# Kernel optimization log

Hardware: AMD Instinct MI355X
Metric: run time of the kernel (lower is better)

Reference implementation:

```python
import jax, jax.numpy as jnp
import numpy as np

B, H, WD, C = 16, 96, 96, 256
WS, SH, NH = 6, 3, 8
N = WS * WS
ALPHA = (2 * 6) ** 0.25  # deepnorm alpha, n_layers=6
SCALE = (C // NH) ** 0.5  # faithful to source: head_dim**0.5 (not **-0.5)
EPS = 1e-5


def _rel_index(ws):
    coords = np.stack(np.meshgrid(np.arange(ws), np.arange(ws), indexing='ij'))  # (2,ws,ws)
    flat = coords.reshape(2, -1)
    rel = (flat[:, :, None] - flat[:, None, :]).transpose(1, 2, 0).copy()
    rel[..., 0] += ws - 1
    rel[..., 1] += ws - 1
    rel[..., 0] *= 2 * ws - 1
    return jnp.asarray(rel.sum(-1))  # (N,N) int


def _attn_mask(h, w, ws, sh):
    img = np.zeros((h, w))
    cnt = 0
    for hs in (slice(0, -ws), slice(-ws, -sh), slice(-sh, None)):
        for wsl in (slice(0, -ws), slice(-ws, -sh), slice(-sh, None)):
            img[hs, wsl] = cnt
            cnt += 1
    win = img.reshape(h // ws, ws, w // ws, ws).transpose(0, 2, 1, 3).reshape(-1, ws * ws)
    diff = win[:, None, :] - win[:, :, None]
    return jnp.asarray(np.where(diff != 0, -100.0, 0.0), jnp.float32)  # (nW,N,N)


def _ln(t, w, b):
    mu = jnp.mean(t, -1, keepdims=True)
    var = jnp.var(t, -1, keepdims=True)
    return (t - mu) * jax.lax.rsqrt(var + EPS) * w + b


def setup_inputs() -> dict:
    key = jax.random.key(0)
    ks = jax.random.split(key, 8)
    d = {
        'x': jax.random.normal(ks[0], (B, H * WD, C), jnp.float32),
        'qkv_w': jax.random.normal(ks[1], (C, 3 * C), jnp.float32) * 0.02,
        'qkv_b': jnp.zeros((3 * C,), jnp.float32),
        'bias_table': jax.random.normal(ks[2], ((2 * WS - 1) ** 2, NH), jnp.float32) * 0.02,
        'proj_w': jax.random.normal(ks[3], (C, C), jnp.float32) * 0.02,
        'proj_b': jnp.zeros((C,), jnp.float32),
        'norm1_w': jnp.ones((C,), jnp.float32),
        'norm1_b': jnp.zeros((C,), jnp.float32),
        'norm2_w': jnp.ones((C,), jnp.float32),
        'norm2_b': jnp.zeros((C,), jnp.float32),
        'fc1_w': jax.random.normal(ks[4], (C, 4 * C), jnp.float32) * 0.02,
        'fc1_b': jnp.zeros((4 * C,), jnp.float32),
        'fc2_w': jax.random.normal(ks[5], (4 * C, C), jnp.float32) * 0.02,
        'fc2_b': jnp.zeros((C,), jnp.float32),
    }
    return d


def reference(x, qkv_w, qkv_b, bias_table, proj_w, proj_b, norm1_w, norm1_b,
              norm2_w, norm2_b, fc1_w, fc1_b, fc2_w, fc2_b):
    hd = C // NH
    nW = (H // WS) * (WD // WS)
    shortcut = x  # (B, L, C), norm_before=False -> post-norm
    xs = x.reshape(B, H, WD, C)
    xs = jnp.roll(xs, (-SH, -SH), axis=(1, 2))  # cyclic shift
    # window partition -> (B*nW, N, C)
    xw = xs.reshape(B, H // WS, WS, WD // WS, WS, C).transpose(0, 1, 3, 2, 4, 5).reshape(B * nW, N, C)
    qkv = (xw @ qkv_w + qkv_b).reshape(B * nW, N, 3, NH, hd).transpose(2, 0, 3, 1, 4)
    q, k, v = qkv[0] * SCALE, qkv[1], qkv[2]
    attn = jnp.einsum('bhnd,bhmd->bhnm', q, k)  # (B*nW, H, N, N)
    bias = bias_table[_rel_index(WS).reshape(-1)].reshape(N, N, NH).transpose(2, 0, 1)
    attn = attn + bias[None]
    mask = _attn_mask(H, WD, WS, SH)  # (nW, N, N)
    attn = attn.reshape(B, nW, NH, N, N) + mask[None, :, None]
    attn = jax.nn.softmax(attn.reshape(B * nW, NH, N, N), axis=-1)
    out = jnp.einsum('bhnm,bhmd->bhnd', attn, v).transpose(0, 2, 1, 3).reshape(B * nW, N, C)
    out = out @ proj_w + proj_b
    # faithful buggy window_reverse: identity permute == plain reshape
    xs = out.reshape(B, H // WS, WS, WD // WS, WS, C).reshape(B, H, WD, C)
    xs = jnp.roll(xs, (SH, SH), axis=(1, 2))
    x1 = _ln(shortcut * ALPHA + xs.reshape(B, H * WD, C), norm1_w, norm1_b)
    hmid = jax.nn.gelu(x1 @ fc1_w + fc1_b, approximate=False)
    x2 = _ln(x1 * ALPHA + (hmid @ fc2_w + fc2_b), norm2_w, norm2_b)
    return x2
```

## Files before the change

### kernel.cpp

```cpp
#include <hip/hip_runtime.h>
#include <math.h>

typedef __bf16 bf16x8 __attribute__((ext_vector_type(8)));
typedef __bf16 bf16x4 __attribute__((ext_vector_type(4)));
typedef short  s16x4  __attribute__((ext_vector_type(4)));
typedef float  f32x4  __attribute__((ext_vector_type(4)));

#define NTOK 147456
#define LTOK 9216
#define ALPHA 1.8612097182041991f
#define QSCALE 5.656854249492380196f
#define MFMA32(a,b,c) __builtin_amdgcn_mfma_f32_16x16x32_bf16((a),(b),(c),0,0,0)
#define SWB(row,kb) ((kb) ^ ((row)&7))

__device__ __forceinline__ f32x4 MFMA16(bf16x4 a, bf16x4 b, f32x4 c) {
#if __has_builtin(__builtin_amdgcn_mfma_f32_16x16x16bf16_1k)
    return __builtin_amdgcn_mfma_f32_16x16x16bf16_1k(*(s16x4*)&a, *(s16x4*)&b, c, 0, 0, 0);
#else
    f32x4 d = c;
    asm volatile("s_nop 1\n\ts_nop 1\n\t"
                 "v_mfma_f32_16x16x16_bf16 %0, %1, %2, %0\n\t"
                 "s_nop 7\n\ts_nop 7"
                 : "+v"(d) : "v"(a), "v"(b));
    return d;
#endif
}

__device__ __forceinline__ float gelu_sig(float x) {
    const float e = __expf(-1.702f * x);
    return x * __builtin_amdgcn_rcpf(1.0f + e);
}

__device__ __forceinline__ void gll16(const void* g, void* l) {
    __builtin_amdgcn_global_load_lds(
        (const __attribute__((address_space(1))) void*)g,
        (__attribute__((address_space(3))) void*)l, 16, 0, 0);
}

__global__ __launch_bounds__(256) void k0_prep(
    const float* __restrict__ qkv_w, const float* __restrict__ proj_w,
    const float* __restrict__ fc1_w, const float* __restrict__ fc2_w,
    const float* __restrict__ bias_table,
    __bf16* __restrict__ qkvT, __bf16* __restrict__ projT,
    __bf16* __restrict__ w1T, __bf16* __restrict__ w2T,
    float* __restrict__ bmask)
{
    const int id = blockIdx.x * 256 + threadIdx.x;
    if (id < 196608) {
        const int o = id >> 8, k = id & 255;
        qkvT[id] = (__bf16)qkv_w[k * 768 + o];
    } else if (id < 262144) {
        const int i = id - 196608, o = i >> 8, k = i & 255;
        projT[i] = (__bf16)proj_w[k * 256 + o];
    } else if (id < 524288) {
        const int i = id - 262144, o = i >> 8, k = i & 255;
        w1T[i] = (__bf16)fc1_w[k * 1024 + o];
    } else if (id < 786432) {
        const int i = id - 524288, o = i >> 10, k = i & 1023;
        w2T[i] = (__bf16)fc2_w[k * 256 + o];
    } else if (id < 860160) {
        const int e = id - 786432;
        const int m = e % 48;
        const int n = (e / 48) % 48;
        const int h = (e / 2304) % 8;
        const int ty = e / 18432;
        const int nn = n < 36 ? n : 35, mm = m < 36 ? m : 35;
        const int i1 = nn / 6, j1 = nn - i1 * 6;
        const int i2 = mm / 6, j2 = mm - i2 * 6;
        float v = bias_table[((i1 - i2 + 5) * 11 + (j1 - j2 + 5)) * 8 + h];
        const int hg1 = (ty & 2) ? (i1 < 3 ? 1 : 2) : 0;
        const int wg1 = (ty & 1) ? (j1 < 3 ? 1 : 2) : 0;
        const int hg2 = (ty & 2) ? (i2 < 3 ? 1 : 2) : 0;
        const int wg2 = (ty & 1) ? (j2 < 3 ? 1 : 2) : 0;
        if (hg1 * 3 + wg1 != hg2 * 3 + wg2) v -= 100.0f;
        if (m >= 36) v = -1e30f;
        bmask[e] = v;
    }
}

__global__ __launch_bounds__(512, 4) void k1f_qkv_attn(
    const float* __restrict__ x, const __bf16* __restrict__ qkvT,
    const float* __restrict__ qkv_b, const float* __restrict__ bmask,
    __bf16* __restrict__ attnout)
{
    __shared__ __attribute__((aligned(16))) __bf16 As[48][256];
    __shared__ int srcrow[48];

    const int t = threadIdx.x;
    const int wid = t >> 6, lane = t & 63;
    const int l15 = lane & 15, lg = lane >> 4;
    const int blk = blockIdx.x;
    const int win = blk & 255;
    const int wh = win >> 4, ww = win & 15;
    const int h = wid;

    if (t < 48) {
        int n = t; if (n > 35) n = 35;
        const int b = blk >> 8;
        const int gh = (wh * 6 + n / 6 + 3) % 96;
        const int gw = (ww * 6 + n % 6 + 3) % 96;
        srcrow[t] = b * LTOK + gh * 96 + gw;
    }
    __syncthreads();

    for (int o = t; o < 48 * 32; o += 512) {
        const int row = o >> 5, kb = o & 31;
        const float* src = x + (size_t)srcrow[row] * 256 + kb * 8;
        const float4 f0 = *(const float4*)src;
        const float4 f1 = *(const float4*)(src + 4);
        bf16x8 p;
        p[0] = (__bf16)f0.x; p[1] = (__bf16)f0.y; p[2] = (__bf16)f0.z; p[3] = (__bf16)f0.w;
        p[4] = (__bf16)f1.x; p[5] = (__bf16)f1.y; p[6] = (__bf16)f1.z; p[7] = (__bf16)f1.w;
        *(bf16x8*)&As[row][SWB(row, kb) * 8] = p;
    }
    __syncthreads();

    const f32x4 fzero = {0.f, 0.f, 0.f, 0.f};
    f32x4 accQ[2][3], accK[2][3], accV[2][3];
    #pragma unroll
    for (int c = 0; c < 2; ++c)
        #pragma unroll
        for (int r = 0; r < 3; ++r) { accQ[c][r] = fzero; accK[c][r] = fzero; accV[c][r] = fzero; }

    const __bf16* bbase = qkvT + (size_t)(h * 32 + l15) * 256 + lg * 8;

    for (int kc = 0; kc < 8; ++kc) {
        bf16x8 af[3];
        #pragma unroll
        for (int rt = 0; rt < 3; ++rt) {
            const int ar = rt * 16 + l15;
            af[rt] = *(const bf16x8*)&As[ar][SWB(ar, kc * 4 + lg) * 8];
        }
        #pragma unroll
        for (int ct = 0; ct < 2; ++ct) {
            const __bf16* bp = bbase + (size_t)ct * 16 * 256 + kc * 32;
            const bf16x8 bq = *(const bf16x8*)bp;
            const bf16x8 bk = *(const bf16x8*)(bp + 65536);
            const bf16x8 bv = *(const bf16x8*)(bp + 131072);
            #pragma unroll
            for (int rt = 0; rt < 3; ++rt) {
                accQ[ct][rt] = MFMA32(bq, af[rt], accQ[ct][rt]);
                accK[ct][rt] = MFMA32(bk, af[rt], accK[ct][rt]);
                accV[ct][rt] = MFMA32(af[rt], bv, accV[ct][rt]);
            }
        }
    }

    bf16x4 qf[3][2], kf[3][2];
    bf16x4 vf[2][3];
    #pragma unroll
    for (int dh = 0; dh < 2; ++dh) {
        #pragma unroll
        for (int q = 0; q < 4; ++q) {
            const float qb = qkv_b[h * 32 + dh * 16 + lg * 4 + q];
            const float kb = qkv_b[256 + h * 32 + dh * 16 + lg * 4 + q];
            #pragma unroll
            for (int rt = 0; rt < 3; ++rt) {
                qf[rt][dh][q] = (__bf16)((accQ[dh][rt][q] + qb) * QSCALE);
                kf[rt][dh][q] = (__bf16)(accK[dh][rt][q] + kb);
            }
        }
    }
    #pragma unroll
    for (int cd = 0; cd < 2; ++cd) {
        const float vb = qkv_b[512 + h * 32 + cd * 16 + l15];
        #pragma unroll
        for (int c3 = 0; c3 < 3; ++c3)
            #pragma unroll
            for (int q = 0; q < 4; ++q)
                vf[cd][c3][q] = (__bf16)(accV[cd][c3][q] + vb);
    }

    f32x4 s[3][3];
    #pragma unroll
    for (int qt = 0; qt < 3; ++qt)
        #pragma unroll
        for (int c3 = 0; c3 < 3; ++c3) {
            f32x4 acc = MFMA16(kf[c3][0], qf[qt][0], fzero);
            s[qt][c3] = MFMA16(kf[c3][1], qf[qt][1], acc);
        }

    const int ty = ((wh == 15) ? 2 : 0) + ((ww == 15) ? 1 : 0);
    const float* bmp = bmask + (size_t)(ty * 8 + h) * 2304;
    bf16x4 pa[3][3];
    #pragma unroll
    for (int qt = 0; qt < 3; ++qt) {
        const float* brow = bmp + (qt * 16 + l15) * 48 + lg * 4;
        const float4 b0 = *(const float4*)brow;
        const float4 b1 = *(const float4*)(brow + 16);
        const float4 b2 = *(const float4*)(brow + 32);
        float vals[3][4];
        #pragma unroll
        for (int q = 0; q < 4; ++q) {
            vals[0][q] = s[qt][0][q] + ((const float*)&b0)[q];
            vals[1][q] = s[qt][1][q] + ((const float*)&b1)[q];
            vals[2][q] = s[qt][2][q] + ((const float*)&b2)[q];
        }
        float mx = -1e30f;
        #pragma unroll
        for (int c3 = 0; c3 < 3; ++c3)
            #pragma unroll
            for (int q = 0; q < 4; ++q) mx = fmaxf(mx, vals[c3][q]);
        mx = fmaxf(mx, __shfl_xor(mx, 16));
        mx = fmaxf(mx, __shfl_xor(mx, 32));
        float sum = 0.f;
        #pragma unroll
        for (int c3 = 0; c3 < 3; ++c3)
            #pragma unroll
            for (int q = 0; q < 4; ++q) {
                const float e = __expf(vals[c3][q] - mx);
                vals[c3][q] = e;
                sum += e;
            }
        sum += __shfl_xor(sum, 16);
        sum += __shfl_xor(sum, 32);
        const float inv = 1.0f / sum;
        #pragma unroll
        for (int c3 = 0; c3 < 3; ++c3)
            #pragma unroll
            for (int q = 0; q < 4; ++q)
                pa[qt][c3][q] = (__bf16)(vals[c3][q] * inv);
    }

    const size_t rowbase = (size_t)blk * 36;
    #pragma unroll
    for (int qt = 0; qt < 3; ++qt)
        #pragma unroll
        for (int cd = 0; cd < 2; ++cd) {
            f32x4 o = MFMA16(pa[qt][0], vf[cd][0], fzero);
            o = MFMA16(pa[qt][1], vf[cd][1], o);
            o = MFMA16(pa[qt][2], vf[cd][2], o);
            #pragma unroll
            for (int q = 0; q < 4; ++q) {
                const int n = qt * 16 + lg * 4 + q;
                if (n < 36)
                    attnout[(rowbase + n) * 256 + h * 32 + cd * 16 + l15] = (__bf16)o[q];
            }
        }
}

__global__ __launch_bounds__(512) void k2_proj_ln(
    const __bf16* __restrict__ attnout, const __bf16* __restrict__ projT,
    const float* __restrict__ proj_b, const float* __restrict__ x,
    const float* __restrict__ n1w, const float* __restrict__ n1b,
    __bf16* __restrict__ x1b)
{
    __shared__ __attribute__((aligned(16))) __bf16 As[128][64];
    __shared__ __attribute__((aligned(16))) __bf16 Bs[256][64];
    __shared__ float ps[128][4], ps2[128][4];
    const int t = threadIdx.x;
    const int wid = t >> 6, lane = t & 63;
    const int l15 = lane & 15, lg = lane >> 4;
    const int mb = blockIdx.x;
    const int wm = wid >> 2, wn = wid & 3;

    const f32x4 fzero = {0.f, 0.f, 0.f, 0.f};
    f32x4 acc[4][4];
    #pragma unroll
    for (int i = 0; i < 4; ++i)
        #pragma unroll
        for (int j = 0; j < 4; ++j) acc[i][j] = fzero;

    for (int kc = 0; kc < 4; ++kc) {
        __syncthreads();
        #pragma unroll
        for (int i = 0; i < 2; ++i) {
            const int r0 = wid * 16 + i * 8;
            const int row = r0 + (lane >> 3), kbl = lane & 7;
            gll16(attnout + (size_t)(mb * 128 + row) * 256 + kc * 64 + ((kbl ^ (row & 7)) * 8),
                  &As[r0][0]);
        }
        #pragma unroll
        for (int i = 0; i < 4; ++i) {
            const int r0 = wid * 32 + i * 8;
            const int row = r0 + (lane >> 3), kbl = lane & 7;
            gll16(projT + (size_t)row * 256 + kc * 64 + ((kbl ^ (row & 7)) * 8),
                  &Bs[r0][0]);
        }
        __syncthreads();
        #pragma unroll
        for (int kk = 0; kk < 2; ++kk) {
            bf16x8 af[4], bfr[4];
            #pragma unroll
            for (int rt = 0; rt < 4; ++rt) {
                const int ar = wm * 64 + rt * 16 + l15;
                af[rt] = *(const bf16x8*)&As[ar][((kk * 4 + lg) ^ (ar & 7)) * 8];
            }
            #pragma unroll
            for (int ct = 0; ct < 4; ++ct) {
                const int br = wn * 64 + ct * 16 + l15;
                bfr[ct] = *(const bf16x8*)&Bs[br][((kk * 4 + lg) ^ (br & 7)) * 8];
            }
            #pragma unroll
            for (int rt = 0; rt < 4; ++rt)
                #pragma unroll
                for (int ct = 0; ct < 4; ++ct)
                    acc[rt][ct] = MFMA32(af[rt], bfr[ct], acc[rt][ct]);
        }
    }

    int dtok_[4][4];
    #pragma unroll
    for (int rt = 0; rt < 4; ++rt) {
        #pragma unroll
        for (int q = 0; q < 4; ++q) {
            const int rowl = wm * 64 + rt * 16 + lg * 4 + q;
            const int tok = mb * 128 + rowl;
            const int b = tok / LTOK, l = tok % LTOK;
            const int hh = l / 96, wwp = l % 96;
            const int dtok = b * LTOK + ((hh + 3) % 96) * 96 + ((wwp + 3) % 96);
            dtok_[rt][q] = dtok;
            float s = 0.f, s2 = 0.f;
            #pragma unroll
            for (int ct = 0; ct < 4; ++ct) {
                const int col = wn * 64 + ct * 16 + l15;
                const float v = acc[rt][ct][q] + proj_b[col] + ALPHA * x[(size_t)dtok * 256 + col];
                acc[rt][ct][q] = v;
                s += v; s2 += v * v;
            }
            s  += __shfl_xor(s, 1, 16);  s += __shfl_xor(s, 2, 16);
            s  += __shfl_xor(s, 4, 16);  s += __shfl_xor(s, 8, 16);
            s2 += __shfl_xor(s2, 1, 16); s2 += __shfl_xor(s2, 2, 16);
            s2 += __shfl_xor(s2, 4, 16); s2 += __shfl_xor(s2, 8, 16);
            if (l15 == 0) { ps[rowl][wn] = s; ps2[rowl][wn] = s2; }
        }
    }
    __syncthreads();
    #pragma unroll
    for (int rt = 0; rt < 4; ++rt) {
        #pragma unroll
        for (int q = 0; q < 4; ++q) {
            const int rowl = wm * 64 + rt * 16 + lg * 4 + q;
            const float S  = ps[rowl][0] + ps[rowl][1] + ps[rowl][2] + ps[rowl][3];
            const float S2 = ps2[rowl][0] + ps2[rowl][1] + ps2[rowl][2] + ps2[rowl][3];
            const float mu = S * (1.0f / 256.0f);
            const float var = S2 * (1.0f / 256.0f) - mu * mu;
            const float rstd = rsqrtf(var + 1e-5f);
            __bf16* op = x1b + (size_t)dtok_[rt][q] * 256;
            #pragma unroll
            for (int ct = 0; ct < 4; ++ct) {
                const int col = wn * 64 + ct * 16 + l15;
                op[col] = (__bf16)((acc[rt][ct][q] - mu) * rstd * n1w[col] + n1b[col]);
            }
        }
    }
}

__global__ __launch_bounds__(256, 2) void k3f_mlp(
    const __bf16* __restrict__ x1b, const __bf16* __restrict__ w1T,
    const float* __restrict__ fc1_b, const __bf16* __restrict__ w2T,
    const float* __restrict__ fc2_b, const float* __restrict__ n2w,
    const float* __restrict__ n2b, float* __restrict__ out)
{
    __shared__ __attribute__((aligned(16))) __bf16 w1c[2][32][256];
    __shared__ __attribute__((aligned(16))) __bf16 w2c[2][256][32];
    __shared__ __attribute__((aligned(16))) __bf16 hs[4][32][32];
    __shared__ float fc1b_s[1024], fc2b_s[256], n2w_s[256], n2b_s[256];

    const int t = threadIdx.x;
    const int wv = t >> 6, lane = t & 63;
    const int l15 = lane & 15, lg = lane >> 4;
    const int rowbase = blockIdx.x * 128 + wv * 32;

    for (int o = t; o < 1024; o += 256) fc1b_s[o] = fc1_b[o];
    if (t < 256) { fc2b_s[t] = fc2_b[t]; n2w_s[t] = n2w[t]; n2b_s[t] = n2b[t]; }

    bf16x8 af[2][8];
    #pragma unroll
    for (int tt = 0; tt < 2; ++tt)
        #pragma unroll
        for (int kk = 0; kk < 8; ++kk)
            af[tt][kk] = *(const bf16x8*)(x1b + (size_t)(rowbase + tt * 16 + l15) * 256 + kk * 32 + lg * 8);

    const f32x4 fzero = {0.f, 0.f, 0.f, 0.f};
    f32x4 acc2[2][16];
    #pragma unroll
    for (int i = 0; i < 2; ++i)
        #pragma unroll
        for (int j = 0; j < 16; ++j) acc2[i][j] = fzero;

    #define STAGE_W(b, c)                                                        \
    {                                                                            \
        _Pragma("unroll")                                                        \
        for (int i = 0; i < 4; ++i) {                                            \
            const int r0 = wv * 8 + i * 2;                                       \
            const int row = r0 + (lane >> 5);                                    \
            const int g = (lane & 31) ^ (row & 7);                               \
            gll16(w1T + (size_t)((c) * 32 + row) * 256 + g * 8, &w1c[b][r0][0]); \
        }                                                                        \
        _Pragma("unroll")                                                        \
        for (int i = 0; i < 4; ++i) {                                            \
            const int r0 = wv * 64 + i * 16;                                     \
            const int row = r0 + (lane >> 2);                                    \
            const int g = (lane & 3) ^ ((row >> 1) & 3);                         \
            gll16(w2T + (size_t)row * 1024 + (c) * 32 + g * 8, &w2c[b][r0][0]);  \
        }                                                                        \
    }

    STAGE_W(0, 0);
    asm volatile("s_waitcnt vmcnt(0)" ::: "memory");
    __builtin_amdgcn_sched_barrier(0);
    __builtin_amdgcn_s_barrier();
    __builtin_amdgcn_sched_barrier(0);

    for (int ch = 0; ch < 32; ++ch) {
        const int cur = ch & 1;
        if (ch < 31) STAGE_W(cur ^ 1, ch + 1);

        f32x4 acc1[2][2];
        #pragma unroll
        for (int i = 0; i < 2; ++i)
            #pragma unroll
            for (int j = 0; j < 2; ++j) acc1[i][j] = fzero;
        __builtin_amdgcn_s_setprio(1);
        #pragma unroll
        for (int kk = 0; kk < 8; ++kk) {
            #pragma unroll
            for (int ht = 0; ht < 2; ++ht) {
                const int hr = ht * 16 + l15;
                const bf16x8 aW = *(const bf16x8*)&w1c[cur][hr][((kk * 4 + lg) ^ (hr & 7)) * 8];
                #pragma unroll
                for (int tt = 0; tt < 2; ++tt)
                    acc1[ht][tt] = MFMA32(aW, af[tt][kk], acc1[ht][tt]);
            }
        }
        __builtin_amdgcn_s_setprio(0);

        #pragma unroll
        for (int ht = 0; ht < 2; ++ht) {
            float bq[4];
            #pragma unroll
            for (int q = 0; q < 4; ++q)
                bq[q] = fc1b_s[ch * 32 + ht * 16 + lg * 4 + q];
            #pragma unroll
            for (int tt = 0; tt < 2; ++tt) {
                bf16x4 p;
                #pragma unroll
                for (int q = 0; q < 4; ++q)
                    p[q] = (__bf16)gelu_sig(acc1[ht][tt][q] + bq[q]);
                const int row = tt * 16 + l15;
                const int gW = ht * 2 + (lg >> 1);
                *(bf16x4*)&hs[wv][row][(gW ^ ((row >> 1) & 3)) * 8 + (lg & 1) * 4] = p;
            }
        }

        bf16x8 a2[2];
        #pragma unroll
        for (int tt = 0; tt < 2; ++tt) {
            const int row = tt * 16 + l15;
            a2[tt] = *(const bf16x8*)&hs[wv][row][((lg ^ ((row >> 1) & 3))) * 8];
        }
        __builtin_amdgcn_s_setprio(1);
        #pragma unroll
        for (int ct = 0; ct < 16; ++ct) {
            const int br = ct * 16 + l15;
            const bf16x8 bW = *(const bf16x8*)&w2c[cur][br][((lg ^ ((br >> 1) & 3))) * 8];
            #pragma unroll
            for (int tt = 0; tt < 2; ++tt)
                acc2[tt][ct] = MFMA32(a2[tt], bW, acc2[tt][ct]);
        }
        __builtin_amdgcn_s_setprio(0);

        asm volatile("s_waitcnt vmcnt(0)" ::: "memory");
        __builtin_amdgcn_sched_barrier(0);
        __builtin_amdgcn_s_barrier();
        __builtin_amdgcn_sched_barrier(0);
    }

    #pragma unroll
    for (int tt = 0; tt < 2; ++tt) {
        #pragma unroll
        for (int q = 0; q < 4; ++q) {
            const int grow = tt * 16 + lg * 4 + q;
            const size_t tok = (size_t)(rowbase + grow);
            float s = 0.f, s2 = 0.f;
            float vals[16];
            #pragma unroll
            for (int ct = 0; ct < 16; ++ct) {
                const int col = ct * 16 + l15;
                const float v = acc2[tt][ct][q] + fc2b_s[col] + ALPHA * (float)x1b[tok * 256 + col];
                vals[ct] = v;
                s += v; s2 += v * v;
            }
            s  += __shfl_xor(s, 1, 16);  s += __shfl_xor(s, 2, 16);
            s  += __shfl_xor(s, 4, 16);  s += __shfl_xor(s, 8, 16);
            s2 += __shfl_xor(s2, 1, 16); s2 += __shfl_xor(s2, 2, 16);
            s2 += __shfl_xor(s2, 4, 16); s2 += __shfl_xor(s2, 8, 16);
            const float mu = s * (1.0f / 256.0f);
            const float var = s2 * (1.0f / 256.0f) - mu * mu;
            const float rstd = rsqrtf(var + 1e-5f);
            float* op = out + tok * 256;
            #pragma unroll
            for (int ct = 0; ct < 16; ++ct) {
                const int col = ct * 16 + l15;
                op[col] = (vals[ct] - mu) * rstd * n2w_s[col] + n2b_s[col];
            }
        }
    }
    #undef STAGE_W
}

extern "C" void kernel_launch(void* const* d_in, const int* in_sizes, int n_in,
                              void* d_out, int out_size, void* d_ws, size_t ws_size,
                              hipStream_t stream)
{
    const float* x          = (const float*)d_in[0];
    const float* qkv_w      = (const float*)d_in[1];
    const float* qkv_b      = (const float*)d_in[2];
    const float* bias_table = (const float*)d_in[3];
    const float* proj_w     = (const float*)d_in[4];
    const float* proj_b     = (const float*)d_in[5];
    const float* n1w        = (const float*)d_in[6];
    const float* n1b        = (const float*)d_in[7];
    const float* n2w        = (const float*)d_in[8];
    const float* n2b        = (const float*)d_in[9];
    const float* fc1_w      = (const float*)d_in[10];
    const float* fc1_b      = (const float*)d_in[11];
    const float* fc2_w      = (const float*)d_in[12];
    const float* fc2_b      = (const float*)d_in[13];
    float* out = (float*)d_out;

    char* ws = (char*)d_ws;
    __bf16* x1b     = (__bf16*)ws;
    __bf16* attnout = (__bf16*)(ws + 75497472);
    __bf16* qkvT    = (__bf16*)(ws + 150994944);
    __bf16* projT   = (__bf16*)(ws + 151388160);
    __bf16* w1T     = (__bf16*)(ws + 151519232);
    __bf16* w2T     = (__bf16*)(ws + 152043520);
    float*  bmask   = (float*)(ws + 152567808);

    k0_prep<<<3360, 256, 0, stream>>>(qkv_w, proj_w, fc1_w, fc2_w, bias_table,
                                      qkvT, projT, w1T, w2T, bmask);
    k1f_qkv_attn<<<4096, 512, 0, stream>>>(x, qkvT, qkv_b, bmask, attnout);
    k2_proj_ln<<<1152, 512, 0, stream>>>(attnout, projT, proj_b, x, n1w, n1b, x1b);
    k3f_mlp<<<1152, 256, 0, stream>>>(x1b, w1T, fc1_b, w2T, fc2_b, n2w, n2b, out);
}
```

Before: 597.4 us.

## Read MLP weights directly from global memory instead of staging through LDS

The MLP kernel stops double-buffering fc1/fc2 weight chunks into shared memory with async global-to-LDS loads and per-chunk barriers. Each wave now loads its MFMA weight fragments straight from global memory, relying on L1/L2 caching since all blocks share the same weights. This removes the per-chunk block barriers and frees about 64KB of LDS, which could allow more waves per CU. The cost is repeated global/L2 traffic per wave and exposed load latency, with no explicit prefetch.

```diff
diff --git a/kernel.cpp b/kernel.cpp
--- a/kernel.cpp
+++ b/kernel.cpp
@@ -352,8 +352,6 @@
     const float* __restrict__ fc2_b, const float* __restrict__ n2w,
     const float* __restrict__ n2b, float* __restrict__ out)
 {
-    __shared__ __attribute__((aligned(16))) __bf16 w1c[2][32][256];
-    __shared__ __attribute__((aligned(16))) __bf16 w2c[2][256][32];
     __shared__ __attribute__((aligned(16))) __bf16 hs[4][32][32];
     __shared__ float fc1b_s[1024], fc2b_s[256], n2w_s[256], n2b_s[256];
 
@@ -364,6 +362,7 @@
 
     for (int o = t; o < 1024; o += 256) fc1b_s[o] = fc1_b[o];
     if (t < 256) { fc2b_s[t] = fc2_b[t]; n2w_s[t] = n2w[t]; n2b_s[t] = n2b[t]; }
+    __syncthreads();
 
     bf16x8 af[2][8];
     #pragma unroll
@@ -379,52 +378,28 @@
         #pragma unroll
         for (int j = 0; j < 16; ++j) acc2[i][j] = fzero;
 
-    #define STAGE_W(b, c)                                                        \
-    {                                                                            \
-        _Pragma("unroll")                                                        \
-        for (int i = 0; i < 4; ++i) {                                            \
-            const int r0 = wv * 8 + i * 2;                                       \
-            const int row = r0 + (lane >> 5);                                    \
-            const int g = (lane & 31) ^ (row & 7);                               \
-            gll16(w1T + (size_t)((c) * 32 + row) * 256 + g * 8, &w1c[b][r0][0]); \
-        }                                                                        \
-        _Pragma("unroll")                                                        \
-        for (int i = 0; i < 4; ++i) {                                            \
-            const int r0 = wv * 64 + i * 16;                                     \
-            const int row = r0 + (lane >> 2);                                    \
-            const int g = (lane & 3) ^ ((row >> 1) & 3);                         \
-            gll16(w2T + (size_t)row * 1024 + (c) * 32 + g * 8, &w2c[b][r0][0]);  \
-        }                                                                        \
-    }
-
-    STAGE_W(0, 0);
-    asm volatile("s_waitcnt vmcnt(0)" ::: "memory");
-    __builtin_amdgcn_sched_barrier(0);
-    __builtin_amdgcn_s_barrier();
-    __builtin_amdgcn_sched_barrier(0);
+    const __bf16* w1base = w1T + (size_t)l15 * 256 + lg * 8;
+    const __bf16* w2base = w2T + (size_t)l15 * 1024 + lg * 8;
 
     for (int ch = 0; ch < 32; ++ch) {
-        const int cur = ch & 1;
-        if (ch < 31) STAGE_W(cur ^ 1, ch + 1);
-
         f32x4 acc1[2][2];
         #pragma unroll
         for (int i = 0; i < 2; ++i)
             #pragma unroll
             for (int j = 0; j < 2; ++j) acc1[i][j] = fzero;
-        __builtin_amdgcn_s_setprio(1);
-        #pragma unroll
-        for (int kk = 0; kk < 8; ++kk) {
-            #pragma unroll
-            for (int ht = 0; ht < 2; ++ht) {
-                const int hr = ht * 16 + l15;
-                const bf16x8 aW = *(const bf16x8*)&w1c[cur][hr][((kk * 4 + lg) ^ (hr & 7)) * 8];
+        #pragma unroll
+        for (int ht = 0; ht < 2; ++ht) {
+            const __bf16* w1p = w1base + (size_t)(ch * 32 + ht * 16) * 256;
+            __builtin_amdgcn_s_setprio(1);
+            #pragma unroll
+            for (int kk = 0; kk < 8; ++kk) {
+                const bf16x8 aW = *(const bf16x8*)(w1p + kk * 32);
                 #pragma unroll
                 for (int tt = 0; tt < 2; ++tt)
                     acc1[ht][tt] = MFMA32(aW, af[tt][kk], acc1[ht][tt]);
             }
-        }
-        __builtin_amdgcn_s_setprio(0);
+            __builtin_amdgcn_s_setprio(0);
+        }
 
         #pragma unroll
         for (int ht = 0; ht < 2; ++ht) {
@@ -450,21 +425,16 @@
             const int row = tt * 16 + l15;
             a2[tt] = *(const bf16x8*)&hs[wv][row][((lg ^ ((row >> 1) & 3))) * 8];
         }
+        const __bf16* w2p = w2base + ch * 32;
         __builtin_amdgcn_s_setprio(1);
         #pragma unroll
         for (int ct = 0; ct < 16; ++ct) {
-            const int br = ct * 16 + l15;
-            const bf16x8 bW = *(const bf16x8*)&w2c[cur][br][((lg ^ ((br >> 1) & 3))) * 8];
+            const bf16x8 bW = *(const bf16x8*)(w2p + (size_t)ct * 16 * 1024);
             #pragma unroll
             for (int tt = 0; tt < 2; ++tt)
                 acc2[tt][ct] = MFMA32(a2[tt], bW, acc2[tt][ct]);
         }
         __builtin_amdgcn_s_setprio(0);
-
-        asm volatile("s_waitcnt vmcnt(0)" ::: "memory");
-        __builtin_amdgcn_sched_barrier(0);
-        __builtin_amdgcn_s_barrier();
-        __builtin_amdgcn_sched_barrier(0);
     }
 
     #pragma unroll
@@ -497,7 +467,6 @@
             }
         }
     }
-    #undef STAGE_W
 }
 
 extern "C" void kernel_launch(void* const* d_in, const int* in_sizes, int n_in,
```

Result: slower. 1.061 ms (+77.6%).
